# Kernel tuning notes

Measured on AMD Instinct MI355X. Metric: run time of the kernel, lower is better.

The kernel has to match this reference:

```python
import jax, jax.numpy as jnp
import numpy as np

B, S, D, H = 8, 1024, 512, 8
HD = D // H
EPS = 1e-5


def layer_norm(x, g, b):
    m = jnp.mean(x, axis=-1, keepdims=True)
    v = jnp.mean(jnp.square(x - m), axis=-1, keepdims=True)
    return (x - m) * jax.lax.rsqrt(v + EPS) * g + b


def mha(x, w_in, b_in, w_out, b_out):
    # x: [B,S,D]; w_in: [3D,D]; PyTorch MultiheadAttention math (no dropout, eval)
    b, s, d = x.shape
    qkv = x @ w_in.T + b_in                      # [B,S,3D]
    q, k, v = jnp.split(qkv, 3, axis=-1)
    q = q.reshape(b, s, H, HD)
    k = k.reshape(b, s, H, HD)
    v = v.reshape(b, s, H, HD)
    scores = jnp.einsum('bqhd,bkhd->bhqk', q, k) / np.sqrt(HD)
    a = jax.nn.softmax(scores, axis=-1)
    o = jnp.einsum('bhqk,bkhd->bqhd', a, v).reshape(b, s, d)
    return o @ w_out.T + b_out


def interp_linear(y, out_size):
    # y: [B,S_in,D]; torch F.interpolate(mode='linear', align_corners=False)
    s_in = y.shape[1]
    scale = s_in / out_size
    src = (jnp.arange(out_size, dtype=jnp.float32) + 0.5) * scale - 0.5
    src = jnp.clip(src, 0.0, s_in - 1.0)
    i0 = jnp.floor(src).astype(jnp.int32)
    i1 = jnp.minimum(i0 + 1, s_in - 1)
    w = (src - i0.astype(jnp.float32))[None, :, None]
    return y[:, i0, :] * (1.0 - w) + y[:, i1, :] * w


def setup_inputs() -> dict:
    key = jax.random.key(0)
    ks = jax.random.split(key, 16)
    sd = 0.02
    return {
        'x': jax.random.normal(ks[0], (B, S, D), jnp.float32),
        'w_in1': jax.random.normal(ks[1], (3 * D, D), jnp.float32) * sd,
        'b_in1': jnp.zeros((3 * D,), jnp.float32),
        'w_out1': jax.random.normal(ks[2], (D, D), jnp.float32) * sd,
        'b_out1': jnp.zeros((D,), jnp.float32),
        'w_in2': jax.random.normal(ks[3], (3 * D, D), jnp.float32) * sd,
        'b_in2': jnp.zeros((3 * D,), jnp.float32),
        'w_out2': jax.random.normal(ks[4], (D, D), jnp.float32) * sd,
        'b_out2': jnp.zeros((D,), jnp.float32),
        'g1': jnp.ones((D,), jnp.float32), 'beta1': jnp.zeros((D,), jnp.float32),
        'g2': jnp.ones((D,), jnp.float32), 'beta2': jnp.zeros((D,), jnp.float32),
        'g3': jnp.ones((D,), jnp.float32), 'beta3': jnp.zeros((D,), jnp.float32),
        'w_ff1': jax.random.normal(ks[5], (4 * D, D), jnp.float32) * sd,
        'b_ff1': jnp.zeros((4 * D,), jnp.float32),
        'w_ff2': jax.random.normal(ks[6], (D, 4 * D), jnp.float32) * sd,
        'b_ff2': jnp.zeros((D,), jnp.float32),
    }


def reference(x, w_in1, b_in1, w_out1, b_out1, w_in2, b_in2, w_out2, b_out2,
              g1, beta1, g2, beta2, g3, beta3, w_ff1, b_ff1, w_ff2, b_ff2):
    a1 = mha(x, w_in1, b_in1, w_out1, b_out1)
    x = layer_norm(x + a1, g1, beta1)
    # avg_pool1d kernel=2 stride=2 ceil_mode (S even -> exact halving)
    pooled = x.reshape(B, S // 2, 2, D).mean(axis=2)
    a2 = mha(pooled, w_in2, b_in2, w_out2, b_out2)
    up = interp_linear(a2, S)
    x = layer_norm(x + up, g2, beta2)
    h = jax.nn.gelu(x @ w_ff1.T + b_ff1, approximate=False)
    ff = h @ w_ff2.T + b_ff2
    return layer_norm(x + ff, g3, beta3)
```

## Files before the change

### kernel.cpp

```cpp
#include <hip/hip_runtime.h>
#include <hip/hip_bf16.h>
#include <math.h>

typedef __hip_bfloat16 bf16;
typedef __attribute__((ext_vector_type(8))) short short8;
typedef __attribute__((ext_vector_type(4))) short s4v;
typedef __attribute__((ext_vector_type(4))) float f32x4;
typedef __attribute__((ext_vector_type(16))) float f32x16;

__device__ __forceinline__ float ldf(const float* p, size_t i) { return p[i]; }
__device__ __forceinline__ float ldf(const bf16*  p, size_t i) { return __bfloat162float(p[i]); }
__device__ __forceinline__ void  stf(float* p, size_t i, float v) { p[i] = v; }
__device__ __forceinline__ void  stf(bf16*  p, size_t i, float v) { p[i] = __float2bfloat16(v); }

__device__ __forceinline__ float ex2(float x) { return __builtin_amdgcn_exp2f(x); }

__device__ __forceinline__ void gl16(const void* gp, void* lp) {
    __builtin_amdgcn_global_load_lds(
        (const __attribute__((address_space(1))) void*)gp,
        (__attribute__((address_space(3))) void*)lp, 16, 0, 0);
}

__device__ __forceinline__ int lof(int row, int bo) {
    return row * 136 + (((bo >> 4) ^ (row & 7)) << 4) + (bo & 15);
}

__device__ __forceinline__ void pl32swap(unsigned &a, unsigned &b) {
    asm volatile("v_permlane32_swap_b32 %0, %1" : "+v"(a), "+v"(b));
}

__global__ __launch_bounds__(256) void cvt_kernel(
    const float* __restrict__ src, bf16* __restrict__ dst, int n)
{
    for (int i = blockIdx.x * 256 + threadIdx.x; i < n; i += gridDim.x * 256)
        dst[i] = __float2bfloat16(src[i]);
}

__global__ __launch_bounds__(256) void cvt_w(
    const float* __restrict__ s0, const float* __restrict__ s1,
    const float* __restrict__ s2, const float* __restrict__ s3,
    const float* __restrict__ s4, const float* __restrict__ s5,
    bf16* __restrict__ dst)
{
    int i = blockIdx.x * 256 + threadIdx.x;
    const float* s; int off;
    if      (i <  786432) { s = s0; off = 0; }
    else if (i < 1048576) { s = s1; off =  786432; }
    else if (i < 1835008) { s = s2; off = 1048576; }
    else if (i < 2097152) { s = s3; off = 1835008; }
    else if (i < 3145728) { s = s4; off = 2097152; }
    else                  { s = s5; off = 3145728; }
    dst[i] = __float2bfloat16(s[i - off]);
}

template <int EPI>
__global__ __launch_bounds__(256) void gemm_mfma(
    const bf16* __restrict__ A, const bf16* __restrict__ W,
    const float* __restrict__ bias, bf16* __restrict__ C,
    int M, int N, int K)
{
    __shared__ __align__(16) bf16 Asl[2][128 * 64];
    __shared__ __align__(16) bf16 Bsl[2][128 * 64];

    const int tid  = threadIdx.x;
    const int lane = tid & 63;
    const int wave = tid >> 6;
    const int wm   = wave >> 1;
    const int wn   = wave & 1;
    const int l15  = lane & 15;
    const int quad = lane >> 4;
    const int sr   = lane >> 3;
    const int sc   = ((lane & 7) ^ sr) * 8;

    const int row0 = blockIdx.y * 128, col0 = blockIdx.x * 128;

    f32x4 acc[4][4] = {};

    const int nk = K >> 6;

    #pragma unroll
    for (int t = 0; t < 4; t++) {
        int r0 = wave * 32 + t * 8;
        gl16(&A[(size_t)(row0 + r0 + sr) * K + sc], &Asl[0][r0 * 64]);
        gl16(&W[(size_t)(col0 + r0 + sr) * K + sc], &Bsl[0][r0 * 64]);
    }

    int cur = 0;
    for (int i = 0; i < nk; i++) {
        __syncthreads();
        if (i + 1 < nk) {
            int k1 = (i + 1) << 6;
            #pragma unroll
            for (int t = 0; t < 4; t++) {
                int r0 = wave * 32 + t * 8;
                gl16(&A[(size_t)(row0 + r0 + sr) * K + k1 + sc], &Asl[cur ^ 1][r0 * 64]);
                gl16(&W[(size_t)(col0 + r0 + sr) * K + k1 + sc], &Bsl[cur ^ 1][r0 * 64]);
            }
        }

        #pragma unroll
        for (int ks = 0; ks < 64; ks += 32) {
            short8 af[4], bfr[4];
            const int g0 = (ks >> 3) + quad;
            const int col = (g0 ^ (l15 & 7)) * 8;
            #pragma unroll
            for (int mt = 0; mt < 4; mt++)
                af[mt] = *(const short8*)&Asl[cur][(wm * 64 + mt * 16 + l15) * 64 + col];
            #pragma unroll
            for (int nt = 0; nt < 4; nt++)
                bfr[nt] = *(const short8*)&Bsl[cur][(wn * 64 + nt * 16 + l15) * 64 + col];
            #pragma unroll
            for (int mt = 0; mt < 4; mt++)
                #pragma unroll
                for (int nt = 0; nt < 4; nt++)
                    acc[mt][nt] = __builtin_amdgcn_mfma_f32_16x16x32_bf16(
                        af[mt], bfr[nt], acc[mt][nt], 0, 0, 0);
        }
        cur ^= 1;
    }

    #pragma unroll
    for (int mt = 0; mt < 4; mt++) {
        int row = row0 + wm * 64 + mt * 16 + quad * 4;
        #pragma unroll
        for (int nt = 0; nt < 4; nt++) {
            int col = col0 + wn * 64 + nt * 16 + l15;
            float bv = bias[col];
            #pragma unroll
            for (int r = 0; r < 4; r++) {
                float v = acc[mt][nt][r] + bv;
                if (EPI == 1) v = 0.5f * v * (1.0f + erff(v * 0.70710678118654752f));
                C[(size_t)(row + r) * N + col] = __float2bfloat16(v);
            }
        }
    }
}

template <int LQB>
__global__ __launch_bounds__(128) void flash_attn_mfma(
    const bf16* __restrict__ qkv, bf16* __restrict__ o)
{
    constexpr int S  = 64 << LQB;
    constexpr int nt = 1 << LQB;

    __shared__ __align__(16) bf16 Kl[64 * 68];
    __shared__ __align__(16) bf16 Vt[64 * 68];
    __shared__ float aB[2][32];

    const int tid  = threadIdx.x;
    const int wave = tid >> 6, lane = tid & 63;
    const int l31  = lane & 31, hi = lane >> 5;

    const int r    = blockIdx.x;
    const int w    = (r & 7) * ((1 << LQB) * 8) + (r >> 3);
    const int qblk = w & ((1 << LQB) - 1);
    const int bh   = w >> LQB;
    const int h    = bh & 7, bb = bh >> 3;
    const int q0   = qblk * 64 + wave * 32;

    const bf16* base = qkv + (size_t)bb * S * 1536 + h * 64;
    char* Kb = (char*)Kl;
    char* Vb = (char*)Vt;

    short8 qf[4];
    #pragma unroll
    for (int c = 0; c < 4; c++)
        qf[c] = *(const short8*)&base[(size_t)(q0 + l31) * 1536 + c * 16 + hi * 8];

    f32x16 oacc[2] = {};
    float m2 = -3.0e38f, lrow = 0.f;
    const float CE = 0.18033688f;

    const int kr  = tid >> 1, kh = tid & 1;
    const int vc0 = (tid & 15) * 4, vr8 = (tid >> 4) * 8;

    short8 kst[4];
    s4v    vst[8];

    auto LOADKV = [&](int k0) {
        #pragma unroll
        for (int i = 0; i < 4; i++)
            kst[i] = *(const short8*)&base[(size_t)(k0 + kr) * 1536 + 512 + kh * 32 + i * 8];
        #pragma unroll
        for (int i = 0; i < 8; i++)
            vst[i] = *(const s4v*)&base[(size_t)(k0 + vr8 + i) * 1536 + 1024 + vc0];
    };

    auto WRITEKV = [&]() {
        #pragma unroll
        for (int i = 0; i < 4; i++) {
            int off = lof(kr, kh * 64 + i * 16);
            *(long*)(Kb + off)     = ((const long*)&kst[i])[0];
            *(long*)(Kb + off + 8) = ((const long*)&kst[i])[1];
        }
        #pragma unroll
        for (int i = 0; i < 4; i++) {
            union { bf16 b[8]; long l[2]; } pk;
            #pragma unroll
            for (int j = 0; j < 8; j++) pk.b[j] = ((const bf16*)&vst[j])[i];
            int off = lof(vc0 + i, vr8 * 2);
            *(long*)(Vb + off)     = pk.l[0];
            *(long*)(Vb + off + 8) = pk.l[1];
        }
    };

    LOADKV(0);
    for (int it = 0; it < nt; it++) {
        __syncthreads();
        WRITEKV();
        __syncthreads();
        if (it + 1 < nt) LOADKV((it + 1) << 6);

        #pragma unroll
        for (int sub = 0; sub < 2; sub++) {
            f32x16 st = {};
            #pragma unroll
            for (int c = 0; c < 4; c++) {
                union { long l[2]; short8 s; } af;
                int off = lof(sub * 32 + l31, c * 32 + hi * 16);
                af.l[0] = *(const long*)(Kb + off);
                af.l[1] = *(const long*)(Kb + off + 8);
                st = __builtin_amdgcn_mfma_f32_32x32x16_bf16(af.s, qf[c], st, 0, 0, 0);
            }

            float cm = st[0];
            #pragma unroll
            for (int r2 = 1; r2 < 16; r2++) cm = fmaxf(cm, st[r2]);
            cm = fmaxf(cm, __shfl_xor(cm, 32));
            float cm2 = cm * CE;

            if (__any(cm2 > m2 + 8.f)) {
                float mn2 = fmaxf(m2, cm2);
                float alpha = ex2(m2 - mn2);
                m2 = mn2; lrow *= alpha;
                if (hi == 0) aB[wave][l31] = alpha;
                #pragma unroll
                for (int r2 = 0; r2 < 16; r2++) {
                    float av = aB[wave][(r2 & 3) + 8 * (r2 >> 2) + 4 * hi];
                    oacc[0][r2] *= av; oacc[1][r2] *= av;
                }
            }

            float p[16]; float ps = 0.f;
            #pragma unroll
            for (int r2 = 0; r2 < 16; r2++) { p[r2] = ex2(st[r2] * CE - m2); ps += p[r2]; }
            ps += __shfl_xor(ps, 32);
            lrow += ps;

            unsigned wk[8];
            #pragma unroll
            for (int j = 0; j < 8; j++)
                asm("v_cvt_pk_bf16_f32 %0, %1, %2" : "=v"(wk[j]) : "v"(p[2*j]), "v"(p[2*j+1]));

            #pragma unroll
            for (int kk = 0; kk < 2; kk++) {
                pl32swap(wk[kk*4+0], wk[kk*4+2]);
                pl32swap(wk[kk*4+1], wk[kk*4+3]);
                union { unsigned u[4]; short8 s; } pa;
                pa.u[0] = wk[kk*4+0]; pa.u[1] = wk[kk*4+1];
                pa.u[2] = wk[kk*4+2]; pa.u[3] = wk[kk*4+3];
                #pragma unroll
                for (int dt = 0; dt < 2; dt++) {
                    union { long l[2]; short8 s; } vf;
                    int off = lof(dt * 32 + l31, sub * 64 + kk * 32 + hi * 16);
                    vf.l[0] = *(const long*)(Vb + off);
                    vf.l[1] = *(const long*)(Vb + off + 8);
                    oacc[dt] = __builtin_amdgcn_mfma_f32_32x32x16_bf16(pa.s, vf.s, oacc[dt], 0, 0, 0);
                }
            }
        }
    }

    if (hi == 0) aB[wave][l31] = 1.0f / lrow;
    #pragma unroll
    for (int r2 = 0; r2 < 16; r2++) {
        int qr = (r2 & 3) + 8 * (r2 >> 2) + 4 * hi;
        float iv = aB[wave][qr];
        size_t rb = ((size_t)bb * S + q0 + qr) * 512 + h * 64;
        o[rb + l31]      = __float2bfloat16(oacc[0][r2] * iv);
        o[rb + 32 + l31] = __float2bfloat16(oacc[1][r2] * iv);
    }
}

template <typename AT, typename OT, bool INTERP>
__global__ __launch_bounds__(256) void ln_kernel(
    const AT* __restrict__ a, const bf16* __restrict__ bsrc,
    const float* __restrict__ g, const float* __restrict__ beta,
    OT* __restrict__ out)
{
    const int row = blockIdx.x;
    const int t = threadIdx.x;
    const size_t base = (size_t)row * 512;

    float a0 = ldf(a, base + t), a1 = ldf(a, base + t + 256);
    float b0, b1;
    if (INTERP) {
        int s = row & 1023, bb = row >> 10;
        float src = fminf(fmaxf((s + 0.5f) * 0.5f - 0.5f, 0.f), 511.f);
        int i0 = (int)src;
        int i1 = min(i0 + 1, 511);
        float w = src - (float)i0;
        size_t r0 = ((size_t)bb * 512 + i0) * 512;
        size_t r1 = ((size_t)bb * 512 + i1) * 512;
        b0 = __bfloat162float(bsrc[r0 + t]) * (1.f - w) + __bfloat162float(bsrc[r1 + t]) * w;
        b1 = __bfloat162float(bsrc[r0 + t + 256]) * (1.f - w) + __bfloat162float(bsrc[r1 + t + 256]) * w;
    } else {
        b0 = __bfloat162float(bsrc[base + t]);
        b1 = __bfloat162float(bsrc[base + t + 256]);
    }
    float v0 = a0 + b0, v1 = a1 + b1;

    __shared__ float red[4];
    const int lane = t & 63, wid = t >> 6;

    float sm = v0 + v1;
    #pragma unroll
    for (int off = 32; off > 0; off >>= 1) sm += __shfl_xor(sm, off);
    if (lane == 0) red[wid] = sm;
    __syncthreads();
    sm = red[0] + red[1] + red[2] + red[3];
    const float mean = sm * (1.0f / 512.0f);

    float d0 = v0 - mean, d1 = v1 - mean;
    float vv = d0 * d0 + d1 * d1;
    __syncthreads();
    #pragma unroll
    for (int off = 32; off > 0; off >>= 1) vv += __shfl_xor(vv, off);
    if (lane == 0) red[wid] = vv;
    __syncthreads();
    vv = red[0] + red[1] + red[2] + red[3];
    const float rstd = rsqrtf(vv * (1.0f / 512.0f) + 1e-5f);

    stf(out, base + t,       d0 * rstd * g[t]       + beta[t]);
    stf(out, base + t + 256, d1 * rstd * g[t + 256] + beta[t + 256]);
}

__global__ __launch_bounds__(256) void pool_kernel(
    const bf16* __restrict__ x, bf16* __restrict__ p)
{
    size_t i = (size_t)blockIdx.x * 256 + threadIdx.x;
    size_t d = i & 511;
    size_t rs = i >> 9;
    size_t b = rs >> 9, s = rs & 511;
    size_t r = (b * 1024 + 2 * s) * 512 + d;
    p[i] = __float2bfloat16(0.5f * (__bfloat162float(x[r]) + __bfloat162float(x[r + 512])));
}

extern "C" void kernel_launch(void* const* d_in, const int* in_sizes, int n_in,
                              void* d_out, int out_size, void* d_ws, size_t ws_size,
                              hipStream_t stream)
{
    const float* x      = (const float*)d_in[0];
    const float* w_in1  = (const float*)d_in[1];
    const float* b_in1  = (const float*)d_in[2];
    const float* w_out1 = (const float*)d_in[3];
    const float* b_out1 = (const float*)d_in[4];
    const float* w_in2  = (const float*)d_in[5];
    const float* b_in2  = (const float*)d_in[6];
    const float* w_out2 = (const float*)d_in[7];
    const float* b_out2 = (const float*)d_in[8];
    const float* g1     = (const float*)d_in[9];
    const float* be1    = (const float*)d_in[10];
    const float* g2     = (const float*)d_in[11];
    const float* be2    = (const float*)d_in[12];
    const float* g3     = (const float*)d_in[13];
    const float* be3    = (const float*)d_in[14];
    const float* w_ff1  = (const float*)d_in[15];
    const float* b_ff1  = (const float*)d_in[16];
    const float* w_ff2  = (const float*)d_in[17];
    const float* b_ff2  = (const float*)d_in[18];

    bf16* ws     = (bf16*)d_ws;
    bf16* xb     = ws + 0;
    bf16* wq1    = ws + 4194304;
    bf16* wo1    = ws + 4980736;
    bf16* wq2    = ws + 5242880;
    bf16* wo2    = ws + 6029312;
    bf16* wf1    = ws + 6291456;
    bf16* wf2    = ws + 7340032;
    bf16* qkv1   = ws + 8388608;
    bf16* o1     = ws + 20971520;
    bf16* a1     = ws + 25165824;
    bf16* x1     = ws + 29360128;
    bf16* pooled = ws + 33554432;
    bf16* qkv2   = ws + 35651584;
    bf16* o2     = ws + 41943040;
    bf16* a2     = ws + 44040192;
    bf16* x2     = ws + 46137344;
    bf16* h      = ws + 8388608;
    bf16* ff     = ws + 25165824;

    dim3 blk(256);
    dim3 fblk(128);

    cvt_kernel<<<4096, blk, 0, stream>>>(x, xb, 4194304);
    cvt_w<<<16384, blk, 0, stream>>>(w_in1, w_out1, w_in2, w_out2, w_ff1, w_ff2, wq1);

    gemm_mfma<0><<<dim3(12, 64), blk, 0, stream>>>(xb, wq1, b_in1, qkv1, 8192, 1536, 512);
    flash_attn_mfma<4><<<dim3(1024), fblk, 0, stream>>>(qkv1, o1);
    gemm_mfma<0><<<dim3(4, 64), blk, 0, stream>>>(o1, wo1, b_out1, a1, 8192, 512, 512);
    ln_kernel<float, bf16, false><<<8192, blk, 0, stream>>>(x, a1, g1, be1, x1);
    pool_kernel<<<8192, blk, 0, stream>>>(x1, pooled);
    gemm_mfma<0><<<dim3(12, 32), blk, 0, stream>>>(pooled, wq2, b_in2, qkv2, 4096, 1536, 512);
    flash_attn_mfma<3><<<dim3(512), fblk, 0, stream>>>(qkv2, o2);
    gemm_mfma<0><<<dim3(4, 32), blk, 0, stream>>>(o2, wo2, b_out2, a2, 4096, 512, 512);
    ln_kernel<bf16, bf16, true><<<8192, blk, 0, stream>>>(x1, a2, g2, be2, x2);
    gemm_mfma<1><<<dim3(16, 64), blk, 0, stream>>>(x2, wf1, b_ff1, h, 8192, 2048, 512);
    gemm_mfma<0><<<dim3(4, 64), blk, 0, stream>>>(h, wf2, b_ff2, ff, 8192, 512, 2048);
    ln_kernel<bf16, float, false><<<8192, blk, 0, stream>>>(x2, ff, g3, be3, (float*)d_out);
}
```

Before: 337.3 us.

## Replace LDS-staged GEMM with direct global-to-register MFMA GEMM

Result: slower. 502.2 us (+48.9%).

```diff
diff --git a/kernel.cpp b/kernel.cpp
--- a/kernel.cpp
+++ b/kernel.cpp
@@ -14,12 +14,6 @@
 __device__ __forceinline__ void  stf(bf16*  p, size_t i, float v) { p[i] = __float2bfloat16(v); }
 
 __device__ __forceinline__ float ex2(float x) { return __builtin_amdgcn_exp2f(x); }
-
-__device__ __forceinline__ void gl16(const void* gp, void* lp) {
-    __builtin_amdgcn_global_load_lds(
-        (const __attribute__((address_space(1))) void*)gp,
-        (__attribute__((address_space(3))) void*)lp, 16, 0, 0);
-}
 
 __device__ __forceinline__ int lof(int row, int bo) {
     return row * 136 + (((bo >> 4) ^ (row & 7)) << 4) + (bo & 15);
@@ -53,78 +47,59 @@
     dst[i] = __float2bfloat16(s[i - off]);
 }
 
-template <int EPI>
-__global__ __launch_bounds__(256) void gemm_mfma(
+template <int NF, int EPI>
+__global__ __launch_bounds__(256) void gemm_direct(
     const bf16* __restrict__ A, const bf16* __restrict__ W,
     const float* __restrict__ bias, bf16* __restrict__ C,
     int M, int N, int K)
 {
-    __shared__ __align__(16) bf16 Asl[2][128 * 64];
-    __shared__ __align__(16) bf16 Bsl[2][128 * 64];
-
     const int tid  = threadIdx.x;
     const int lane = tid & 63;
     const int wave = tid >> 6;
-    const int wm   = wave >> 1;
-    const int wn   = wave & 1;
-    const int l15  = lane & 15;
-    const int quad = lane >> 4;
-    const int sr   = lane >> 3;
-    const int sc   = ((lane & 7) ^ sr) * 8;
-
-    const int row0 = blockIdx.y * 128, col0 = blockIdx.x * 128;
-
-    f32x4 acc[4][4] = {};
-
-    const int nk = K >> 6;
-
-    #pragma unroll
-    for (int t = 0; t < 4; t++) {
-        int r0 = wave * 32 + t * 8;
-        gl16(&A[(size_t)(row0 + r0 + sr) * K + sc], &Asl[0][r0 * 64]);
-        gl16(&W[(size_t)(col0 + r0 + sr) * K + sc], &Bsl[0][r0 * 64]);
-    }
-
-    int cur = 0;
-    for (int i = 0; i < nk; i++) {
-        __syncthreads();
-        if (i + 1 < nk) {
-            int k1 = (i + 1) << 6;
-            #pragma unroll
-            for (int t = 0; t < 4; t++) {
-                int r0 = wave * 32 + t * 8;
-                gl16(&A[(size_t)(row0 + r0 + sr) * K + k1 + sc], &Asl[cur ^ 1][r0 * 64]);
-                gl16(&W[(size_t)(col0 + r0 + sr) * K + k1 + sc], &Bsl[cur ^ 1][r0 * 64]);
-            }
-        }
-
-        #pragma unroll
-        for (int ks = 0; ks < 64; ks += 32) {
-            short8 af[4], bfr[4];
-            const int g0 = (ks >> 3) + quad;
-            const int col = (g0 ^ (l15 & 7)) * 8;
-            #pragma unroll
-            for (int mt = 0; mt < 4; mt++)
-                af[mt] = *(const short8*)&Asl[cur][(wm * 64 + mt * 16 + l15) * 64 + col];
-            #pragma unroll
-            for (int nt = 0; nt < 4; nt++)
-                bfr[nt] = *(const short8*)&Bsl[cur][(wn * 64 + nt * 16 + l15) * 64 + col];
-            #pragma unroll
-            for (int mt = 0; mt < 4; mt++)
-                #pragma unroll
-                for (int nt = 0; nt < 4; nt++)
-                    acc[mt][nt] = __builtin_amdgcn_mfma_f32_16x16x32_bf16(
-                        af[mt], bfr[nt], acc[mt][nt], 0, 0, 0);
-        }
-        cur ^= 1;
+    const int wm   = wave >> 1, wn = wave & 1;
+    const int l15  = lane & 15, quad = lane >> 4;
+
+    const int row0 = blockIdx.y * 128 + wm * 64;
+    const int col0 = blockIdx.x * (NF * 32) + wn * (NF * 16);
+
+    const bf16* Ab = &A[(size_t)(row0 + l15) * K + quad * 8];
+    const bf16* Wb = &W[(size_t)(col0 + l15) * K + quad * 8];
+
+    f32x4 acc[4][NF] = {};
+    short8 a0[4], b0[NF], a1[4], b1[NF];
+
+    auto LD = [&](short8 (&aa)[4], short8 (&bb)[NF], int kk) {
+        #pragma unroll
+        for (int mt = 0; mt < 4; mt++)
+            aa[mt] = *(const short8*)&Ab[(size_t)(mt * 16) * K + kk];
+        #pragma unroll
+        for (int nt = 0; nt < NF; nt++)
+            bb[nt] = *(const short8*)&Wb[(size_t)(nt * 16) * K + kk];
+    };
+    auto MM = [&](short8 (&aa)[4], short8 (&bb)[NF]) {
+        #pragma unroll
+        for (int mt = 0; mt < 4; mt++)
+            #pragma unroll
+            for (int nt = 0; nt < NF; nt++)
+                acc[mt][nt] = __builtin_amdgcn_mfma_f32_16x16x32_bf16(
+                    aa[mt], bb[nt], acc[mt][nt], 0, 0, 0);
+    };
+
+    const int nk = K >> 5;
+    LD(a0, b0, 0);
+    for (int k = 0; k < nk; k += 2) {
+        LD(a1, b1, (k + 1) << 5);
+        MM(a0, b0);
+        if (k + 2 < nk) LD(a0, b0, (k + 2) << 5);
+        MM(a1, b1);
     }
 
     #pragma unroll
     for (int mt = 0; mt < 4; mt++) {
-        int row = row0 + wm * 64 + mt * 16 + quad * 4;
-        #pragma unroll
-        for (int nt = 0; nt < 4; nt++) {
-            int col = col0 + wn * 64 + nt * 16 + l15;
+        int row = row0 + mt * 16 + quad * 4;
+        #pragma unroll
+        for (int nt = 0; nt < NF; nt++) {
+            int col = col0 + nt * 16 + l15;
             float bv = bias[col];
             #pragma unroll
             for (int r = 0; r < 4; r++) {
@@ -396,16 +371,16 @@
     cvt_kernel<<<4096, blk, 0, stream>>>(x, xb, 4194304);
     cvt_w<<<16384, blk, 0, stream>>>(w_in1, w_out1, w_in2, w_out2, w_ff1, w_ff2, wq1);
 
-    gemm_mfma<0><<<dim3(12, 64), blk, 0, stream>>>(xb, wq1, b_in1, qkv1, 8192, 1536, 512);
+    gemm_direct<4,0><<<dim3(12, 64), blk, 0, stream>>>(xb, wq1, b_in1, qkv1, 8192, 1536, 512);
     flash_attn_mfma<4><<<dim3(1024), fblk, 0, stream>>>(qkv1, o1);
-    gemm_mfma<0><<<dim3(4, 64), blk, 0, stream>>>(o1, wo1, b_out1, a1, 8192, 512, 512);
+    gemm_direct<2,0><<<dim3(8, 64), blk, 0, stream>>>(o1, wo1, b_out1, a1, 8192, 512, 512);
     ln_kernel<float, bf16, false><<<8192, blk, 0, stream>>>(x, a1, g1, be1, x1);
     pool_kernel<<<8192, blk, 0, stream>>>(x1, pooled);
-    gemm_mfma<0><<<dim3(12, 32), blk, 0, stream>>>(pooled, wq2, b_in2, qkv2, 4096, 1536, 512);
+    gemm_direct<2,0><<<dim3(24, 32), blk, 0, stream>>>(pooled, wq2, b_in2, qkv2, 4096, 1536, 512);
     flash_attn_mfma<3><<<dim3(512), fblk, 0, stream>>>(qkv2, o2);
-    gemm_mfma<0><<<dim3(4, 32), blk, 0, stream>>>(o2, wo2, b_out2, a2, 4096, 512, 512);
+    gemm_direct<2,0><<<dim3(8, 32), blk, 0, stream>>>(o2, wo2, b_out2, a2, 4096, 512, 512);
     ln_kernel<bf16, bf16, true><<<8192, blk, 0, stream>>>(x1, a2, g2, be2, x2);
-    gemm_mfma<1><<<dim3(16, 64), blk, 0, stream>>>(x2, wf1, b_ff1, h, 8192, 2048, 512);
-    gemm_mfma<0><<<dim3(4, 64), blk, 0, stream>>>(h, wf2, b_ff2, ff, 8192, 512, 2048);
+    gemm_direct<4,1><<<dim3(16, 64), blk, 0, stream>>>(x2, wf1, b_ff1, h, 8192, 2048, 512);
+    gemm_direct<2,0><<<dim3(8, 64), blk, 0, stream>>>(h, wf2, b_ff2, ff, 8192, 512, 2048);
     ln_kernel<bf16, float, false><<<8192, blk, 0, stream>>>(x2, ff, g3, be3, (float*)d_out);
 }
```

## Add 256x256-tile GEMM kernel for QKV1 and FF1 projections

Applied to the files above, without the earlier changes.

Result: no change. 341.7 us (+1.3%).

```diff
diff --git a/kernel.cpp b/kernel.cpp
--- a/kernel.cpp
+++ b/kernel.cpp
@@ -122,6 +122,88 @@
     #pragma unroll
     for (int mt = 0; mt < 4; mt++) {
         int row = row0 + wm * 64 + mt * 16 + quad * 4;
+        #pragma unroll
+        for (int nt = 0; nt < 4; nt++) {
+            int col = col0 + wn * 64 + nt * 16 + l15;
+            float bv = bias[col];
+            #pragma unroll
+            for (int r = 0; r < 4; r++) {
+                float v = acc[mt][nt][r] + bv;
+                if (EPI == 1) v = 0.5f * v * (1.0f + erff(v * 0.70710678118654752f));
+                C[(size_t)(row + r) * N + col] = __float2bfloat16(v);
+            }
+        }
+    }
+}
+
+template <int EPI>
+__global__ __launch_bounds__(512, 2) void gemm256(
+    const bf16* __restrict__ A, const bf16* __restrict__ W,
+    const float* __restrict__ bias, bf16* __restrict__ C,
+    int M, int N, int K)
+{
+    __shared__ __align__(16) bf16 Asl[2][256 * 64];
+    __shared__ __align__(16) bf16 Bsl[2][256 * 64];
+
+    const int tid  = threadIdx.x;
+    const int lane = tid & 63;
+    const int wave = tid >> 6;
+    const int wm   = wave >> 2;
+    const int wn   = wave & 3;
+    const int l15  = lane & 15;
+    const int quad = lane >> 4;
+    const int sr   = lane >> 3;
+    const int sc   = ((lane & 7) ^ sr) * 8;
+
+    const int nwg = gridDim.x * gridDim.y;
+    const int bid = blockIdx.y * gridDim.x + blockIdx.x;
+    const int wid = (bid & 7) * (nwg >> 3) + (bid >> 3);
+    const int bx  = wid % gridDim.x, by = wid / gridDim.x;
+
+    const int row0 = by * 256, col0 = bx * 256;
+
+    f32x4 acc[8][4] = {};
+    const int nk = K >> 6;
+
+    #define STG(buf, k0)                                                        \
+        _Pragma("unroll")                                                       \
+        for (int j = 0; j < 4; j++) {                                           \
+            int r0 = j * 64 + (wave << 3);                    \
+            gl16(&A[(size_t)(row0 + r0 + sr) * K + (k0) + sc], &Asl[buf][r0 * 64]); \
+            gl16(&W[(size_t)(col0 + r0 + sr) * K + (k0) + sc], &Bsl[buf][r0 * 64]); \
+        }
+
+    STG(0, 0)
+    int cur = 0;
+    for (int i = 0; i < nk; i++) {
+        __syncthreads();
+        if (i + 1 < nk) { STG(cur ^ 1, (i + 1) << 6) }
+
+        #pragma unroll
+        for (int ks = 0; ks < 64; ks += 32) {
+            short8 af[8], bfr[4];
+            const int g0 = (ks >> 3) + quad;
+            const int col = (g0 ^ (l15 & 7)) * 8;
+            #pragma unroll
+            for (int mt = 0; mt < 8; mt++)
+                af[mt] = *(const short8*)&Asl[cur][(wm * 128 + mt * 16 + l15) * 64 + col];
+            #pragma unroll
+            for (int nt = 0; nt < 4; nt++)
+                bfr[nt] = *(const short8*)&Bsl[cur][(wn * 64 + nt * 16 + l15) * 64 + col];
+            #pragma unroll
+            for (int mt = 0; mt < 8; mt++)
+                #pragma unroll
+                for (int nt = 0; nt < 4; nt++)
+                    acc[mt][nt] = __builtin_amdgcn_mfma_f32_16x16x32_bf16(
+                        af[mt], bfr[nt], acc[mt][nt], 0, 0, 0);
+        }
+        cur ^= 1;
+    }
+    #undef STG
+
+    #pragma unroll
+    for (int mt = 0; mt < 8; mt++) {
+        int row = row0 + wm * 128 + mt * 16 + quad * 4;
         #pragma unroll
         for (int nt = 0; nt < 4; nt++) {
             int col = col0 + wn * 64 + nt * 16 + l15;
@@ -392,11 +474,12 @@
 
     dim3 blk(256);
     dim3 fblk(128);
+    dim3 gblk(512);
 
     cvt_kernel<<<4096, blk, 0, stream>>>(x, xb, 4194304);
     cvt_w<<<16384, blk, 0, stream>>>(w_in1, w_out1, w_in2, w_out2, w_ff1, w_ff2, wq1);
 
-    gemm_mfma<0><<<dim3(12, 64), blk, 0, stream>>>(xb, wq1, b_in1, qkv1, 8192, 1536, 512);
+    gemm256<0><<<dim3(6, 32), gblk, 0, stream>>>(xb, wq1, b_in1, qkv1, 8192, 1536, 512);
     flash_attn_mfma<4><<<dim3(1024), fblk, 0, stream>>>(qkv1, o1);
     gemm_mfma<0><<<dim3(4, 64), blk, 0, stream>>>(o1, wo1, b_out1, a1, 8192, 512, 512);
     ln_kernel<float, bf16, false><<<8192, blk, 0, stream>>>(x, a1, g1, be1, x1);
@@ -405,7 +488,7 @@
     flash_attn_mfma<3><<<dim3(512), fblk, 0, stream>>>(qkv2, o2);
     gemm_mfma<0><<<dim3(4, 32), blk, 0, stream>>>(o2, wo2, b_out2, a2, 4096, 512, 512);
     ln_kernel<bf16, bf16, true><<<8192, blk, 0, stream>>>(x1, a2, g2, be2, x2);
-    gemm_mfma<1><<<dim3(16, 64), blk, 0, stream>>>(x2, wf1, b_ff1, h, 8192, 2048, 512);
+    gemm256<1><<<dim3(8, 32), gblk, 0, stream>>>(x2, wf1, b_ff1, h, 8192, 2048, 512);
     gemm_mfma<0><<<dim3(4, 64), blk, 0, stream>>>(h, wf2, b_ff2, ff, 8192, 512, 2048);
     ln_kernel<bf16, float, false><<<8192, blk, 0, stream>>>(x2, ff, g3, be3, (float*)d_out);
 }
```
